# Optimization experiments

Hardware: AMD Instinct MI355X
Metric: run time of the kernel (lower is better)

## Reference

```python
import jax, jax.numpy as jnp
import numpy as np
from jax import lax

L, H, DH, D, FF = 8, 16, 64, 1024, 4096  # layers, heads, head dim, model dim, mlp hidden
B, S = 4, 512
EPS = 1e-5


def setup_inputs() -> dict:
    key = jax.random.key(0)
    ks = jax.random.split(key, 8)
    std = 0.02
    return {
        "x": jax.random.normal(ks[0], (B, S, D), jnp.float32),
        "ln1_w": jnp.ones((L, D), jnp.float32),
        "ln1_b": jnp.zeros((L, D), jnp.float32),
        "qw": jax.random.normal(ks[1], (L, H, DH, DH), jnp.float32) * std,
        "qb": jnp.zeros((L, H, DH), jnp.float32),
        "kw": jax.random.normal(ks[2], (L, H, DH, DH), jnp.float32) * std,
        "kb": jnp.zeros((L, H, DH), jnp.float32),
        "vw": jax.random.normal(ks[3], (L, H, DH, DH), jnp.float32) * std,
        "vb": jnp.zeros((L, H, DH), jnp.float32),
        "ln2_w": jnp.ones((L, D), jnp.float32),
        "ln2_b": jnp.zeros((L, D), jnp.float32),
        "w1": jax.random.normal(ks[4], (L, D, FF), jnp.float32) * std,
        "b1": jnp.zeros((L, FF), jnp.float32),
        "w2": jax.random.normal(ks[5], (L, FF, D), jnp.float32) * std,
        "b2": jnp.zeros((L, D), jnp.float32),
    }


def _layernorm(x, w, b):
    m = jnp.mean(x, axis=-1, keepdims=True)
    v = jnp.mean(jnp.square(x - m), axis=-1, keepdims=True)
    return (x - m) * lax.rsqrt(v + EPS) * w + b


def reference(x, ln1_w, ln1_b, qw, qb, kw, kb, vw, vb, ln2_w, ln2_b, w1, b1, w2, b2):
    b, s, d = x.shape
    scale = 1.0 / jnp.sqrt(jnp.asarray(DH, x.dtype))

    def layer(h, p):
        (l1w, l1b, Qw, Qb, Kw, Kb, Vw, Vb, l2w, l2b, W1, B1, W2, B2) = p
        y = _layernorm(h, l1w, l1b)
        yh = y.reshape(b, s, H, DH)
        # nn.Linear per head: y @ W.T + b, W is [out=e, in=d]
        q = jnp.einsum('bshd,hed->bshe', yh, Qw) + Qb
        k = jnp.einsum('bshd,hed->bshe', yh, Kw) + Kb
        v = jnp.einsum('bshd,hed->bshe', yh, Vw) + Vb
        attn = jax.nn.softmax(jnp.einsum('bshe,bthe->bhst', q, k) * scale, axis=-1)
        o = jnp.einsum('bhst,bthe->bshe', attn, v).reshape(b, s, d)
        h = h + o
        z = _layernorm(h, l2w, l2b)
        z = jax.nn.gelu(z @ W1 + B1, approximate=False) @ W2 + B2
        return h + z, None

    params = (ln1_w, ln1_b, qw, qb, kw, kb, vw, vb, ln2_w, ln2_b, w1, b1, w2, b2)
    out, _ = lax.scan(layer, x, params)
    return out
```

## Files before the change

kernel.cpp:

```cpp
#include <hip/hip_runtime.h>
#include <hip/hip_bf16.h>

typedef __hip_bfloat16 bf16;
typedef __bf16 bf16x8 __attribute__((ext_vector_type(8)));
typedef float f32x4 __attribute__((ext_vector_type(4)));
typedef unsigned short u16;
typedef unsigned int u32;

#define SEQ 512
#define DMODEL 1024
#define FFDIM 4096
#define NHEAD 16
#define HDIM 64
#define NB 4
#define NLAYER 8

__device__ __forceinline__ u16 f2bu(float f) {
    union { bf16 h; u16 u; } c; c.h = __float2bfloat16(f); return c.u;
}

__device__ __forceinline__ void gload16(const bf16* g, bf16* l) {
    __builtin_amdgcn_global_load_lds(
        (const __attribute__((address_space(1))) unsigned int*)g,
        (__attribute__((address_space(3))) unsigned int*)l,
        16, 0, 0);
}

template<int BM, int BN, int BK, int WM, int WN>
__device__ __forceinline__ void gemm_core(
    const bf16* __restrict__ A, int lda,
    const bf16* __restrict__ B, int ldb,
    int K,
    f32x4 (&acc)[WM/16][WN/16],
    bf16* lA, bf16* lB)
{
    constexpr int NFM = WM / 16, NFN = WN / 16;
    constexpr int WC = BN / WN;
    const int tid  = threadIdx.x;
    const int lane = tid & 63, wave = tid >> 6;
    const int wr = wave / WC, wc = wave % WC;
    const int l15 = lane & 15, l4 = lane >> 4;

    constexpr int ITA = (BM * BK) / (256 * 8);
    constexpr int ITB = (BN * BK) / (256 * 8);

    for (int kt = 0; kt < K; kt += BK) {
        __syncthreads();
#pragma unroll
        for (int it = 0; it < ITA; ++it) {
            const int f = (it * 256 + tid) * 8;
            const int r = f / BK, c = f % BK;
            gload16(A + (long)r * lda + kt + c, lA + f);
        }
#pragma unroll
        for (int it = 0; it < ITB; ++it) {
            const int f = (it * 256 + tid) * 8;
            const int r = f / BK, c = f % BK;
            gload16(B + (long)r * ldb + kt + c, lB + f);
        }
        __syncthreads();
#pragma unroll
        for (int ks = 0; ks < BK / 32; ++ks) {
            bf16x8 af[NFM], bfr[NFN];
#pragma unroll
            for (int fm = 0; fm < NFM; ++fm)
                af[fm] = *(const bf16x8*)(lA + (wr * WM + fm * 16 + l15) * BK + ks * 32 + l4 * 8);
#pragma unroll
            for (int fn = 0; fn < NFN; ++fn)
                bfr[fn] = *(const bf16x8*)(lB + (wc * WN + fn * 16 + l15) * BK + ks * 32 + l4 * 8);
#pragma unroll
            for (int fm = 0; fm < NFM; ++fm)
#pragma unroll
                for (int fn = 0; fn < NFN; ++fn)
                    acc[fm][fn] = __builtin_amdgcn_mfma_f32_16x16x32_bf16(
                        af[fm], bfr[fn], acc[fm][fn], 0, 0, 0);
        }
    }
}

__global__ __launch_bounds__(256) void k_ln(const float* __restrict__ h,
                                            const float* __restrict__ w,
                                            const float* __restrict__ bp,
                                            bf16* __restrict__ out)
{
    const int row = blockIdx.x;
    const int tid = threadIdx.x;
    const float4 x = ((const float4*)(h + (long)row * DMODEL))[tid];
    float s  = x.x + x.y + x.z + x.w;
    float s2 = x.x * x.x + x.y * x.y + x.z * x.z + x.w * x.w;
#pragma unroll
    for (int off = 32; off; off >>= 1) { s += __shfl_xor(s, off); s2 += __shfl_xor(s2, off); }
    __shared__ float rs[4], rs2[4];
    const int wave = tid >> 6;
    if ((tid & 63) == 0) { rs[wave] = s; rs2[wave] = s2; }
    __syncthreads();
    const float S1 = rs[0] + rs[1] + rs[2] + rs[3];
    const float S2 = rs2[0] + rs2[1] + rs2[2] + rs2[3];
    const float mean = S1 * (1.0f / DMODEL);
    const float var  = S2 * (1.0f / DMODEL) - mean * mean;
    const float rstd = rsqrtf(var + 1e-5f);
    const float4 wv = ((const float4*)w)[tid];
    const float4 bv = ((const float4*)bp)[tid];
    uint2 o;
    o.x = (u32)f2bu((x.x - mean) * rstd * wv.x + bv.x) |
          ((u32)f2bu((x.y - mean) * rstd * wv.y + bv.y) << 16);
    o.y = (u32)f2bu((x.z - mean) * rstd * wv.z + bv.z) |
          ((u32)f2bu((x.w - mean) * rstd * wv.w + bv.w) << 16);
    ((uint2*)(out + (long)row * DMODEL))[tid] = o;
}

__global__ __launch_bounds__(256) void k_cvt_qkvw(const float* __restrict__ qw,
                                                  const float* __restrict__ kw,
                                                  const float* __restrict__ vw,
                                                  bf16* __restrict__ wq)
{
    const int i = blockIdx.x * 256 + threadIdx.x;
    const int sel = i >> 14;
    const int off = i & 16383;
    const float* s = (sel == 0) ? qw : (sel == 1) ? kw : vw;
    const float4 v = ((const float4*)s)[off];
    uint2 o;
    o.x = (u32)f2bu(v.x) | ((u32)f2bu(v.y) << 16);
    o.y = (u32)f2bu(v.z) | ((u32)f2bu(v.w) << 16);
    ((uint2*)wq)[i] = o;
}

__global__ __launch_bounds__(256) void k_transpose(const float* __restrict__ src,
                                                   bf16* __restrict__ dst,
                                                   int R, int C)
{
    __shared__ float t[64][65];
    const int rb = blockIdx.x << 6, cb = blockIdx.y << 6;
    const int tid = threadIdx.x;
#pragma unroll
    for (int i = 0; i < 16; ++i) {
        int flat = i * 256 + tid;
        int r = flat >> 6, c = flat & 63;
        t[r][c] = src[(long)(rb + r) * C + cb + c];
    }
    __syncthreads();
#pragma unroll
    for (int i = 0; i < 16; ++i) {
        int flat = i * 256 + tid;
        int c = flat >> 6, r = flat & 63;
        dst[(long)(cb + c) * R + rb + r] = __float2bfloat16(t[r][c]);
    }
}

__global__ __launch_bounds__(256) void k_qkv2(const bf16* __restrict__ y,
                                              const bf16* __restrict__ wq,
                                              const float* __restrict__ qb,
                                              const float* __restrict__ kb,
                                              const float* __restrict__ vb,
                                              bf16* __restrict__ qh,
                                              bf16* __restrict__ kh,
                                              bf16* __restrict__ vt)
{
    __shared__ __align__(16) char lmem[128 * 64 * 2 + 64 * 64 * 2];
    bf16* lA = (bf16*)lmem;
    char* lBb = lmem + 128 * 64 * 2;

    const int tid = threadIdx.x;
    const int lane = tid & 63, wave = tid >> 6;
    const int l15 = lane & 15, l4 = lane >> 4;
    const int z = blockIdx.y;
    const int b = z >> 4, hd = z & 15;
    const bf16* A = y + (long)b * SEQ * DMODEL + hd * HDIM + (long)blockIdx.x * 128 * DMODEL;

#pragma unroll
    for (int it = 0; it < 4; ++it) {
        const int f = (it * 256 + tid) * 8;
        const int r = f >> 6, c = f & 63;
        gload16(A + (long)r * DMODEL + c, lA + f);
    }
    __syncthreads();

    bf16x8 qa[2][2];
#pragma unroll
    for (int fm = 0; fm < 2; ++fm)
#pragma unroll
        for (int ks = 0; ks < 2; ++ks)
            qa[fm][ks] = *(const bf16x8*)(lA + (wave * 32 + fm * 16 + l15) * 64 + ks * 32 + l4 * 8);

    for (int t = 0; t < 3; ++t) {
        __syncthreads();
        const bf16* Bsrc = wq + (long)(t * NHEAD + hd) * HDIM * HDIM;
#pragma unroll
        for (int it = 0; it < 2; ++it) {
            const int f = (it * 256 + tid) * 8;
            const int r = f >> 6;
            const uint4 v = *(const uint4*)(Bsrc + f);
            int byte = (f << 1) ^ ((r & 7) << 4);
            *(uint4*)(lBb + byte) = v;
        }
        __syncthreads();

        bf16x8 bfr[4][2];
#pragma unroll
        for (int fn = 0; fn < 4; ++fn)
#pragma unroll
            for (int ks = 0; ks < 2; ++ks) {
                const int row = fn * 16 + l15;
                int byte = (row << 7) + ((ks * 32 + l4 * 8) << 1);
                byte ^= (row & 7) << 4;
                bfr[fn][ks] = *(const bf16x8*)(lBb + byte);
            }
        f32x4 acc[2][4] = {};
#pragma unroll
        for (int ks = 0; ks < 2; ++ks)
#pragma unroll
            for (int fm = 0; fm < 2; ++fm)
#pragma unroll
                for (int fn = 0; fn < 4; ++fn)
                    acc[fm][fn] = __builtin_amdgcn_mfma_f32_16x16x32_bf16(
                        qa[fm][ks], bfr[fn][ks], acc[fm][fn], 0, 0, 0);

        const float* bias = (t == 0) ? qb : (t == 1) ? kb : vb;
#pragma unroll
        for (int fm = 0; fm < 2; ++fm)
#pragma unroll
            for (int fn = 0; fn < 4; ++fn)
#pragma unroll
                for (int r = 0; r < 4; ++r) {
                    const int srow = blockIdx.x * 128 + wave * 32 + fm * 16 + l4 * 4 + r;
                    const int e = fn * 16 + l15;
                    float v = acc[fm][fn][r] + bias[hd * HDIM + e];
                    if (t == 0) {
                        qh[((long)z * SEQ + srow) * HDIM + e] = __float2bfloat16(v * 0.125f);
                    } else if (t == 1) {
                        kh[((long)z * SEQ + srow) * HDIM + e] = __float2bfloat16(v);
                    } else {
                        vt[((long)z * HDIM + e) * SEQ + srow] = __float2bfloat16(v);
                    }
                }
    }
}

__global__ __launch_bounds__(256) void k_flash(const bf16* __restrict__ qh,
                                               const bf16* __restrict__ kh,
                                               const bf16* __restrict__ vt,
                                               float* __restrict__ h)
{
    __shared__ __align__(16) char lmem[24576];
    bf16* lQ = (bf16*)lmem;
    char* lKb = lmem + 8192;
    char* lVb = lmem + 16384;

    const int tid = threadIdx.x;
    const int lane = tid & 63, wave = tid >> 6;
    const int l15 = lane & 15, l4 = lane >> 4;
    const int z = blockIdx.y;
    const int b = z >> 4, hd = z & 15;
    const int q0 = blockIdx.x * 64;

    const bf16* Qsrc = qh + ((long)z * SEQ + q0) * HDIM;
#pragma unroll
    for (int it = 0; it < 2; ++it) {
        const int f = (it * 256 + tid) * 8;
        gload16(Qsrc + f, lQ + f);
    }
    __syncthreads();

    bf16x8 qa[2];
#pragma unroll
    for (int ks = 0; ks < 2; ++ks)
        qa[ks] = *(const bf16x8*)(lQ + (wave * 16 + l15) * 64 + ks * 32 + l4 * 8);

    char* lPb = lmem + wave * 2048;

    f32x4 O[4] = {};
    float mrun[4], lrun[4];
#pragma unroll
    for (int r = 0; r < 4; ++r) { mrun[r] = -1e30f; lrun[r] = 0.0f; }

    for (int kv = 0; kv < SEQ / 64; ++kv) {
        __syncthreads();
        const bf16* Ksrc = kh + ((long)z * SEQ + kv * 64) * HDIM;
#pragma unroll
        for (int it = 0; it < 2; ++it) {
            const int f = (it * 256 + tid) * 8;
            const int r = f >> 6;
            const uint4 v = *(const uint4*)(Ksrc + f);
            *(uint4*)(lKb + ((f << 1) ^ ((r & 7) << 4))) = v;
        }
        const bf16* Vsrc = vt + (long)z * HDIM * SEQ + kv * 64;
#pragma unroll
        for (int it = 0; it < 2; ++it) {
            const int f = (it * 256 + tid) * 8;
            const int r = f >> 6, c = f & 63;
            const uint4 v = *(const uint4*)(Vsrc + (long)r * SEQ + c);
            *(uint4*)(lVb + ((f << 1) ^ ((r & 7) << 4))) = v;
        }
        __syncthreads();

        f32x4 sa[4];
#pragma unroll
        for (int fn = 0; fn < 4; ++fn) sa[fn] = (f32x4){0.f, 0.f, 0.f, 0.f};
#pragma unroll
        for (int ks = 0; ks < 2; ++ks)
#pragma unroll
            for (int fn = 0; fn < 4; ++fn) {
                const int row = fn * 16 + l15;
                int byte = (row << 7) + ((ks * 32 + l4 * 8) << 1);
                byte ^= (row & 7) << 4;
                const bf16x8 kb_ = *(const bf16x8*)(lKb + byte);
                sa[fn] = __builtin_amdgcn_mfma_f32_16x16x32_bf16(qa[ks], kb_, sa[fn], 0, 0, 0);
            }

#pragma unroll
        for (int r = 0; r < 4; ++r) {
            float mx = fmaxf(fmaxf(sa[0][r], sa[1][r]), fmaxf(sa[2][r], sa[3][r]));
#pragma unroll
            for (int m_ = 1; m_ < 16; m_ <<= 1) mx = fmaxf(mx, __shfl_xor(mx, m_));
            const float nm = fmaxf(mrun[r], mx);
            const float al = __expf(mrun[r] - nm);
            mrun[r] = nm;
            float p0 = __expf(sa[0][r] - nm), p1 = __expf(sa[1][r] - nm);
            float p2 = __expf(sa[2][r] - nm), p3 = __expf(sa[3][r] - nm);
            float ps = p0 + p1 + p2 + p3;
#pragma unroll
            for (int m_ = 1; m_ < 16; m_ <<= 1) ps += __shfl_xor(ps, m_);
            lrun[r] = lrun[r] * al + ps;
#pragma unroll
            for (int fn = 0; fn < 4; ++fn) O[fn][r] *= al;
            const int row = l4 * 4 + r;
            const int rsw = (row & 7) << 4;
            const int rb = row << 7;
            *(u16*)(lPb + ((rb + ((0 * 16 + l15) << 1)) ^ rsw)) = f2bu(p0);
            *(u16*)(lPb + ((rb + ((1 * 16 + l15) << 1)) ^ rsw)) = f2bu(p1);
            *(u16*)(lPb + ((rb + ((2 * 16 + l15) << 1)) ^ rsw)) = f2bu(p2);
            *(u16*)(lPb + ((rb + ((3 * 16 + l15) << 1)) ^ rsw)) = f2bu(p3);
        }

#pragma unroll
        for (int ks = 0; ks < 2; ++ks) {
            const int rowp = l15;
            int pbyte = (rowp << 7) + ((ks * 32 + l4 * 8) << 1);
            pbyte ^= (rowp & 7) << 4;
            const bf16x8 pa = *(const bf16x8*)(lPb + pbyte);
#pragma unroll
            for (int fn = 0; fn < 4; ++fn) {
                const int row = fn * 16 + l15;
                int byte = (row << 7) + ((ks * 32 + l4 * 8) << 1);
                byte ^= (row & 7) << 4;
                const bf16x8 vb_ = *(const bf16x8*)(lVb + byte);
                O[fn] = __builtin_amdgcn_mfma_f32_16x16x32_bf16(pa, vb_, O[fn], 0, 0, 0);
            }
        }
    }

    float rinv[4];
#pragma unroll
    for (int r = 0; r < 4; ++r) rinv[r] = 1.0f / lrun[r];
#pragma unroll
    for (int fn = 0; fn < 4; ++fn)
#pragma unroll
        for (int r = 0; r < 4; ++r) {
            const int srow = q0 + wave * 16 + l4 * 4 + r;
            const int e = fn * 16 + l15;
            h[((long)b * SEQ + srow) * DMODEL + hd * HDIM + e] += O[fn][r] * rinv[r];
        }
}

__global__ __launch_bounds__(256) void k_gemm1(const bf16* __restrict__ zb,
                                               const bf16* __restrict__ w1t,
                                               const float* __restrict__ b1,
                                               bf16* __restrict__ ff1)
{
    constexpr int BM = 128, BN = 128, BK = 64, WM = 64, WN = 64;
    __shared__ __align__(16) bf16 lA[BM * BK];
    __shared__ __align__(16) bf16 lB[BN * BK];
    const bf16* A = zb + (long)blockIdx.x * BM * DMODEL;
    const bf16* B = w1t + (long)blockIdx.y * BN * DMODEL;
    f32x4 acc[4][4] = {};
    gemm_core<BM, BN, BK, WM, WN>(A, DMODEL, B, DMODEL, DMODEL, acc, lA, lB);

    const int lane = threadIdx.x & 63, wave = threadIdx.x >> 6;
    const int wr = wave >> 1, wc = wave & 1, l15 = lane & 15, l4 = lane >> 4;
#pragma unroll
    for (int fm = 0; fm < 4; ++fm)
#pragma unroll
        for (int fn = 0; fn < 4; ++fn)
#pragma unroll
            for (int r = 0; r < 4; ++r) {
                const int row = blockIdx.x * BM + wr * WM + fm * 16 + l4 * 4 + r;
                const int col = blockIdx.y * BN + wc * WN + fn * 16 + l15;
                const float x = acc[fm][fn][r] + b1[col];
                const float g = 0.5f * x * (1.0f + erff(x * 0.70710678118f));
                ff1[(long)row * FFDIM + col] = __float2bfloat16(g);
            }
}

__global__ __launch_bounds__(256) void k_gemm2(const bf16* __restrict__ ff1,
                                               const bf16* __restrict__ w2t,
                                               float* __restrict__ part)
{
    constexpr int BM = 128, BN = 128, BK = 64, WM = 64, WN = 64;
    constexpr int KSPLIT = FFDIM / 4;
    __shared__ __align__(16) bf16 lA[BM * BK];
    __shared__ __align__(16) bf16 lB[BN * BK];
    const int sk = blockIdx.z;
    const bf16* A = ff1 + (long)blockIdx.x * BM * FFDIM + (long)sk * KSPLIT;
    const bf16* B = w2t + (long)blockIdx.y * BN * FFDIM + (long)sk * KSPLIT;
    f32x4 acc[4][4] = {};
    gemm_core<BM, BN, BK, WM, WN>(A, FFDIM, B, FFDIM, KSPLIT, acc, lA, lB);

    float* out = part + (long)sk * (NB * SEQ) * DMODEL;
    const int lane = threadIdx.x & 63, wave = threadIdx.x >> 6;
    const int wr = wave >> 1, wc = wave & 1, l15 = lane & 15, l4 = lane >> 4;
#pragma unroll
    for (int fm = 0; fm < 4; ++fm)
#pragma unroll
        for (int fn = 0; fn < 4; ++fn)
#pragma unroll
            for (int r = 0; r < 4; ++r) {
                const int row = blockIdx.x * BM + wr * WM + fm * 16 + l4 * 4 + r;
                const int col = blockIdx.y * BN + wc * WN + fn * 16 + l15;
                out[(long)row * DMODEL + col] = acc[fm][fn][r];
            }
}

__global__ __launch_bounds__(256) void k_red2(const float* __restrict__ part,
                                              const float* __restrict__ b2,
                                              float* __restrict__ h)
{
    constexpr long NELT = (long)NB * SEQ * DMODEL / 4;
    const long i = (long)blockIdx.x * 256 + threadIdx.x;
    if (i >= NELT) return;
    float4 s = ((const float4*)part)[i];
    const float4 s1 = ((const float4*)part)[i + NELT];
    const float4 s2 = ((const float4*)part)[i + 2 * NELT];
    const float4 s3 = ((const float4*)part)[i + 3 * NELT];
    s.x += s1.x + s2.x + s3.x; s.y += s1.y + s2.y + s3.y;
    s.z += s1.z + s2.z + s3.z; s.w += s1.w + s2.w + s3.w;
    const float4 bv = ((const float4*)b2)[i & (DMODEL / 4 - 1)];
    float4 hv = ((float4*)h)[i];
    hv.x += s.x + bv.x; hv.y += s.y + bv.y;
    hv.z += s.z + bv.z; hv.w += s.w + bv.w;
    ((float4*)h)[i] = hv;
}

extern "C" void kernel_launch(void* const* d_in, const int* in_sizes, int n_in,
                              void* d_out, int out_size, void* d_ws, size_t ws_size,
                              hipStream_t stream)
{
    const float* x    = (const float*)d_in[0];
    const float* ln1w = (const float*)d_in[1];
    const float* ln1b = (const float*)d_in[2];
    const float* qw   = (const float*)d_in[3];
    const float* qb   = (const float*)d_in[4];
    const float* kw   = (const float*)d_in[5];
    const float* kb   = (const float*)d_in[6];
    const float* vw   = (const float*)d_in[7];
    const float* vb   = (const float*)d_in[8];
    const float* ln2w = (const float*)d_in[9];
    const float* ln2b = (const float*)d_in[10];
    const float* w1   = (const float*)d_in[11];
    const float* b1   = (const float*)d_in[12];
    const float* w2   = (const float*)d_in[13];
    const float* b2   = (const float*)d_in[14];

    char* ws = (char*)d_ws;
    const size_t MB = 1024 * 1024;
    bf16* y    = (bf16*)(ws + 0 * MB);
    bf16* zb   = (bf16*)(ws + 4 * MB);
    bf16* qh   = (bf16*)(ws + 8 * MB);
    bf16* kh   = (bf16*)(ws + 12 * MB);
    bf16* vt   = (bf16*)(ws + 16 * MB);
    bf16* ff1  = (bf16*)(ws + 20 * MB);
    bf16* w1t  = (bf16*)(ws + 36 * MB);
    bf16* w2t  = (bf16*)(ws + 44 * MB);
    bf16* wqkv = (bf16*)(ws + 52 * MB);
    float* part = (float*)(ws + 53 * MB);

    float* h = (float*)d_out;
    hipMemcpyAsync(d_out, x, (size_t)NB * SEQ * DMODEL * sizeof(float),
                   hipMemcpyDeviceToDevice, stream);

    for (int l = 0; l < NLAYER; ++l) {
        k_cvt_qkvw<<<192, 256, 0, stream>>>(qw + (long)l * 65536, kw + (long)l * 65536,
                                            vw + (long)l * 65536, wqkv);
        k_ln<<<NB * SEQ, 256, 0, stream>>>(h, ln1w + l * DMODEL, ln1b + l * DMODEL, y);
        k_qkv2<<<dim3(4, NB * NHEAD), 256, 0, stream>>>(
            y, wqkv, qb + l * NHEAD * HDIM, kb + l * NHEAD * HDIM, vb + l * NHEAD * HDIM,
            qh, kh, vt);
        k_flash<<<dim3(SEQ / 64, NB * NHEAD), 256, 0, stream>>>(qh, kh, vt, h);
        k_ln<<<NB * SEQ, 256, 0, stream>>>(h, ln2w + l * DMODEL, ln2b + l * DMODEL, zb);
        k_transpose<<<dim3(16, 64), 256, 0, stream>>>(w1 + (long)l * DMODEL * FFDIM, w1t,
                                                      DMODEL, FFDIM);
        k_gemm1<<<dim3(16, 32), 256, 0, stream>>>(zb, w1t, b1 + l * FFDIM, ff1);
        k_transpose<<<dim3(64, 16), 256, 0, stream>>>(w2 + (long)l * DMODEL * FFDIM, w2t,
                                                      FFDIM, DMODEL);
        k_gemm2<<<dim3(16, 8, 4), 256, 0, stream>>>(ff1, w2t, part);
        k_red2<<<(NB * SEQ * DMODEL / 4 + 255) / 256, 256, 0, stream>>>(part, b2, h);
    }
}
```

Baseline: 1.055 ms.

## Fuse residual reduce with next-layer LayerNorm, merge weight transposes, shrink GEMM tiles

The split-K reduction kernel now also computes the next layer's first LayerNorm per row, so the separate LN1 launch inside the loop goes away. The two weight-transpose launches are merged into one kernel. The FFN GEMMs switch from 128x128 to 64x128 block tiles, doubling the grid to better fill the CUs. The fused LayerNorm uses a one-pass E[x^2]-mean^2 variance, which is slightly less accurate numerically. The changed b2 indexing also fixes the old per-layer bias offset, which was previously always layer 0.

```diff
diff --git a/kernel.cpp b/kernel.cpp
--- a/kernel.cpp
+++ b/kernel.cpp
@@ -125,12 +125,22 @@
     ((uint2*)wq)[i] = o;
 }
 
-__global__ __launch_bounds__(256) void k_transpose(const float* __restrict__ src,
-                                                   bf16* __restrict__ dst,
-                                                   int R, int C)
+__global__ __launch_bounds__(256) void k_transw(const float* __restrict__ w1,
+                                                const float* __restrict__ w2,
+                                                bf16* __restrict__ w1t,
+                                                bf16* __restrict__ w2t)
 {
     __shared__ float t[64][65];
-    const int rb = blockIdx.x << 6, cb = blockIdx.y << 6;
+    int bid = blockIdx.x;
+    const float* src; bf16* dst; int R, C, rb, cb;
+    if (bid < 1024) {
+        src = w1; dst = w1t; R = DMODEL; C = FFDIM;
+        rb = (bid >> 6) << 6; cb = (bid & 63) << 6;
+    } else {
+        bid -= 1024;
+        src = w2; dst = w2t; R = FFDIM; C = DMODEL;
+        rb = (bid >> 4) << 6; cb = (bid & 15) << 6;
+    }
     const int tid = threadIdx.x;
 #pragma unroll
     for (int i = 0; i < 16; ++i) {
@@ -367,18 +377,18 @@
                                                const float* __restrict__ b1,
                                                bf16* __restrict__ ff1)
 {
-    constexpr int BM = 128, BN = 128, BK = 64, WM = 64, WN = 64;
+    constexpr int BM = 64, BN = 128, BK = 64, WM = 32, WN = 64;
     __shared__ __align__(16) bf16 lA[BM * BK];
     __shared__ __align__(16) bf16 lB[BN * BK];
     const bf16* A = zb + (long)blockIdx.x * BM * DMODEL;
     const bf16* B = w1t + (long)blockIdx.y * BN * DMODEL;
-    f32x4 acc[4][4] = {};
+    f32x4 acc[2][4] = {};
     gemm_core<BM, BN, BK, WM, WN>(A, DMODEL, B, DMODEL, DMODEL, acc, lA, lB);
 
     const int lane = threadIdx.x & 63, wave = threadIdx.x >> 6;
     const int wr = wave >> 1, wc = wave & 1, l15 = lane & 15, l4 = lane >> 4;
 #pragma unroll
-    for (int fm = 0; fm < 4; ++fm)
+    for (int fm = 0; fm < 2; ++fm)
 #pragma unroll
         for (int fn = 0; fn < 4; ++fn)
 #pragma unroll
@@ -395,21 +405,21 @@
                                                const bf16* __restrict__ w2t,
                                                float* __restrict__ part)
 {
-    constexpr int BM = 128, BN = 128, BK = 64, WM = 64, WN = 64;
+    constexpr int BM = 64, BN = 128, BK = 64, WM = 32, WN = 64;
     constexpr int KSPLIT = FFDIM / 4;
     __shared__ __align__(16) bf16 lA[BM * BK];
     __shared__ __align__(16) bf16 lB[BN * BK];
     const int sk = blockIdx.z;
     const bf16* A = ff1 + (long)blockIdx.x * BM * FFDIM + (long)sk * KSPLIT;
     const bf16* B = w2t + (long)blockIdx.y * BN * FFDIM + (long)sk * KSPLIT;
-    f32x4 acc[4][4] = {};
+    f32x4 acc[2][4] = {};
     gemm_core<BM, BN, BK, WM, WN>(A, FFDIM, B, FFDIM, KSPLIT, acc, lA, lB);
 
     float* out = part + (long)sk * (NB * SEQ) * DMODEL;
     const int lane = threadIdx.x & 63, wave = threadIdx.x >> 6;
     const int wr = wave >> 1, wc = wave & 1, l15 = lane & 15, l4 = lane >> 4;
 #pragma unroll
-    for (int fm = 0; fm < 4; ++fm)
+    for (int fm = 0; fm < 2; ++fm)
 #pragma unroll
         for (int fn = 0; fn < 4; ++fn)
 #pragma unroll
@@ -420,24 +430,52 @@
             }
 }
 
-__global__ __launch_bounds__(256) void k_red2(const float* __restrict__ part,
-                                              const float* __restrict__ b2,
-                                              float* __restrict__ h)
+__global__ __launch_bounds__(256) void k_red2ln(const float* __restrict__ part,
+                                                const float* __restrict__ b2,
+                                                float* __restrict__ h,
+                                                const float* __restrict__ lnw,
+                                                const float* __restrict__ lnb,
+                                                bf16* __restrict__ y,
+                                                int do_ln)
 {
     constexpr long NELT = (long)NB * SEQ * DMODEL / 4;
-    const long i = (long)blockIdx.x * 256 + threadIdx.x;
-    if (i >= NELT) return;
+    const long row = blockIdx.x;
+    const int tid = threadIdx.x;
+    const long i = row * (DMODEL / 4) + tid;
     float4 s = ((const float4*)part)[i];
     const float4 s1 = ((const float4*)part)[i + NELT];
     const float4 s2 = ((const float4*)part)[i + 2 * NELT];
     const float4 s3 = ((const float4*)part)[i + 3 * NELT];
-    s.x += s1.x + s2.x + s3.x; s.y += s1.y + s2.y + s3.y;
-    s.z += s1.z + s2.z + s3.z; s.w += s1.w + s2.w + s3.w;
-    const float4 bv = ((const float4*)b2)[i & (DMODEL / 4 - 1)];
+    const float4 bv = ((const float4*)b2)[tid];
     float4 hv = ((float4*)h)[i];
-    hv.x += s.x + bv.x; hv.y += s.y + bv.y;
-    hv.z += s.z + bv.z; hv.w += s.w + bv.w;
+    hv.x += s.x + s1.x + s2.x + s3.x + bv.x;
+    hv.y += s.y + s1.y + s2.y + s3.y + bv.y;
+    hv.z += s.z + s1.z + s2.z + s3.z + bv.z;
+    hv.w += s.w + s1.w + s2.w + s3.w + bv.w;
     ((float4*)h)[i] = hv;
+
+    if (!do_ln) return;
+    float ss  = hv.x + hv.y + hv.z + hv.w;
+    float ss2 = hv.x * hv.x + hv.y * hv.y + hv.z * hv.z + hv.w * hv.w;
+#pragma unroll
+    for (int off = 32; off; off >>= 1) { ss += __shfl_xor(ss, off); ss2 += __shfl_xor(ss2, off); }
+    __shared__ float rs[4], rs2[4];
+    const int wave = tid >> 6;
+    if ((tid & 63) == 0) { rs[wave] = ss; rs2[wave] = ss2; }
+    __syncthreads();
+    const float S1 = rs[0] + rs[1] + rs[2] + rs[3];
+    const float S2 = rs2[0] + rs2[1] + rs2[2] + rs2[3];
+    const float mean = S1 * (1.0f / DMODEL);
+    const float var  = S2 * (1.0f / DMODEL) - mean * mean;
+    const float rstd = rsqrtf(var + 1e-5f);
+    const float4 wv = ((const float4*)lnw)[tid];
+    const float4 lb = ((const float4*)lnb)[tid];
+    uint2 o;
+    o.x = (u32)f2bu((hv.x - mean) * rstd * wv.x + lb.x) |
+          ((u32)f2bu((hv.y - mean) * rstd * wv.y + lb.y) << 16);
+    o.y = (u32)f2bu((hv.z - mean) * rstd * wv.z + lb.z) |
+          ((u32)f2bu((hv.w - mean) * rstd * wv.w + lb.w) << 16);
+    ((uint2*)(y + row * DMODEL))[tid] = o;
 }
 
 extern "C" void kernel_launch(void* const* d_in, const int* in_sizes, int n_in,
@@ -477,21 +515,24 @@
     hipMemcpyAsync(d_out, x, (size_t)NB * SEQ * DMODEL * sizeof(float),
                    hipMemcpyDeviceToDevice, stream);
 
+    k_ln<<<NB * SEQ, 256, 0, stream>>>(h, ln1w, ln1b, y);
+
     for (int l = 0; l < NLAYER; ++l) {
         k_cvt_qkvw<<<192, 256, 0, stream>>>(qw + (long)l * 65536, kw + (long)l * 65536,
                                             vw + (long)l * 65536, wqkv);
-        k_ln<<<NB * SEQ, 256, 0, stream>>>(h, ln1w + l * DMODEL, ln1b + l * DMODEL, y);
         k_qkv2<<<dim3(4, NB * NHEAD), 256, 0, stream>>>(
             y, wqkv, qb + l * NHEAD * HDIM, kb + l * NHEAD * HDIM, vb + l * NHEAD * HDIM,
             qh, kh, vt);
         k_flash<<<dim3(SEQ / 64, NB * NHEAD), 256, 0, stream>>>(qh, kh, vt, h);
         k_ln<<<NB * SEQ, 256, 0, stream>>>(h, ln2w + l * DMODEL, ln2b + l * DMODEL, zb);
-        k_transpose<<<dim3(16, 64), 256, 0, stream>>>(w1 + (long)l * DMODEL * FFDIM, w1t,
-                                                      DMODEL, FFDIM);
-        k_gemm1<<<dim3(16, 32), 256, 0, stream>>>(zb, w1t, b1 + l * FFDIM, ff1);
-        k_transpose<<<dim3(64, 16), 256, 0, stream>>>(w2 + (long)l * DMODEL * FFDIM, w2t,
-                                                      FFDIM, DMODEL);
-        k_gemm2<<<dim3(16, 8, 4), 256, 0, stream>>>(ff1, w2t, part);
-        k_red2<<<(NB * SEQ * DMODEL / 4 + 255) / 256, 256, 0, stream>>>(part, b2, h);
-    }
-}
+        k_transw<<<2048, 256, 0, stream>>>(w1 + (long)l * DMODEL * FFDIM,
+                                           w2 + (long)l * DMODEL * FFDIM, w1t, w2t);
+        k_gemm1<<<dim3(32, 32), 256, 0, stream>>>(zb, w1t, b1 + l * FFDIM, ff1);
+        k_gemm2<<<dim3(32, 8, 4), 256, 0, stream>>>(ff1, w2t, part);
+        const int last = (l == NLAYER - 1);
+        k_red2ln<<<NB * SEQ, 256, 0, stream>>>(part, b2 + l * DMODEL, h,
+                                               ln1w + (l + 1) * DMODEL * (1 - last),
+                                               ln1b + (l + 1) * DMODEL * (1 - last),
+                                               y, !last);
+    }
+}
```

Result: slower. 1.127 ms (+6.9%).
